# Performance work log

Hardware: AMD Instinct MI355X
Metric: run time of the kernel (lower is better)

The kernel has to match this reference:

```python
import jax, jax.numpy as jnp
import numpy as np

INPUT_DIM = 362
HIDDEN = 256
STYLE_NUM = 60
OUTFIT_NUM = 49710
BATCH = 16384


def setup_inputs() -> dict:
    key = jax.random.key(0)
    ks = jax.random.split(key, 12)
    f32 = jnp.float32
    return {
        "i_feature": jax.random.normal(ks[0], (BATCH, INPUT_DIM), f32),
        "j_feature": jax.random.normal(ks[1], (BATCH, INPUT_DIM), f32),
        "k_feature": jax.random.normal(ks[2], (BATCH, INPUT_DIM), f32),
        # top_emb / bottom_emb Linear params (stored transposed: x @ W + b)
        "W_top": jax.random.normal(ks[3], (INPUT_DIM, HIDDEN), f32) * 0.05,
        "b_top": jnp.zeros((HIDDEN,), f32),
        "W_bot": jax.random.normal(ks[4], (INPUT_DIM, HIDDEN), f32) * 0.05,
        "b_bot": jnp.zeros((HIDDEN,), f32),
        # NMF factors (forward relu_'s them in place; we relu on use)
        "P_nmf": jax.random.normal(ks[5], (2 * INPUT_DIM, STYLE_NUM), f32),
        "N_nmf": jax.random.normal(ks[6], (2 * INPUT_DIM, STYLE_NUM), f32),
        "H1_nmf": jax.random.normal(ks[7], (STYLE_NUM, OUTFIT_NUM), f32),
        "H2_nmf": jax.random.normal(ks[8], (STYLE_NUM, OUTFIT_NUM), f32),
        "matirx_pos": jax.random.uniform(ks[9], (2 * INPUT_DIM, OUTFIT_NUM), f32),
        "matirx_neg": jax.random.uniform(ks[10], (2 * INPUT_DIM, OUTFIT_NUM), f32),
    }


def _emb(x, W, b):
    # nn.Sequential(Linear, Sigmoid)
    return jax.nn.sigmoid(x @ W + b)


def _style_score(i_f, j_f, styles, W_top, b_top, W_bot, b_bot):
    # Vectorized version of the per-sample loop:
    # squared-distance argmin codebook lookup + gather + rowwise dot.
    outfit = jnp.concatenate([i_f, j_f], axis=1)  # [B, 2D]
    # mean over feature dim of (x - s)^2; constant 1/(2D) scale does not change argmin
    d2 = (jnp.sum(outfit * outfit, axis=1, keepdims=True)
          - 2.0 * (outfit @ styles)
          + jnp.sum(styles * styles, axis=0, keepdims=True))  # [B, S]
    idx = jnp.argmin(d2, axis=1)                               # [B]
    sel = styles.T[idx]                                        # [B, 2D] gather
    top, bot = sel[:, :INPUT_DIM], sel[:, INPUT_DIM:]
    # diag(matmul) == rowwise dot
    return jnp.sum(_emb(top, W_top, b_top) * _emb(bot, W_bot, b_bot), axis=1)  # [B]


def reference(i_feature, j_feature, k_feature, W_top, b_top, W_bot, b_bot,
              P_nmf, N_nmf, H1_nmf, H2_nmf, matirx_pos, matirx_neg):
    Ti = _emb(i_feature, W_top, b_top)   # [B, H]
    Bj = _emb(j_feature, W_bot, b_bot)   # [B, H]
    Bk = _emb(k_feature, W_bot, b_bot)   # [B, H]
    # torch.diag(matmul(Ti, Bj.T)) == rowwise dot (avoids [B,B] intermediate)
    ij_score = jnp.sum(Ti * Bj, axis=1)  # [B]
    ik_score = jnp.sum(Ti * Bk, axis=1)  # [B]

    # forward does relu_ on .data before use
    P = jnp.maximum(P_nmf, 0.0)
    N = jnp.maximum(N_nmf, 0.0)
    H1 = jnp.maximum(H1_nmf, 0.0)
    H2 = jnp.maximum(H2_nmf, 0.0)

    style_ij = _style_score(i_feature, j_feature, P, W_top, b_top, W_bot, b_bot)
    style_ik = _style_score(i_feature, k_feature, N, W_top, b_top, W_bot, b_bot)

    # -mean(log(sigmoid(d))) computed stably
    loss1 = -jnp.mean(jax.nn.log_sigmoid(ij_score - ik_score))
    loss2 = -jnp.mean(jax.nn.log_sigmoid(style_ij - style_ik))
    loss3 = jnp.mean(jnp.square(matirx_pos - P @ H1)
                     + jnp.square(matirx_neg - N @ H2))
    loss = loss1 + loss2 + 0.1 * loss3

    ij_ik = jnp.stack([ij_score, ik_score], axis=1)  # [B, 2]
    auc = jnp.mean((jnp.argmax(ij_ik, axis=1) == 0).astype(jnp.float32))
    return (loss, loss1, loss2, loss3, auc)
```

## Files before the change

### kernel.cpp

```cpp
#include <hip/hip_runtime.h>
#include <math.h>

#define BATCH 16384
#define IND   362
#define KP    384
#define HID   256
#define STY   60
#define NOUT  49710
#define OUTP  49920
#define D2    724
#define D2P   768

#define NB_SS   120
#define NB_HR   3120
#define NB_CW   768
#define NB_CPN  384
#define NB_CF   9216
#define NB_PREP (NB_SS + NB_HR + NB_CW + NB_CPN + NB_CF)

#define NB_HH   16
#define NB_PPB  2
#define NB_HEAD (NB_HH + NB_PPB)
#define N_DT    46
#define N_OC    24
#define OCHUNK  2080
#define NB_M    (2 * N_DT * N_OC)
#define NB_EMB  1024
#define NB_SA   512
#define NB_MAIN (NB_HEAD + NB_M + NB_EMB + NB_SA)

typedef __bf16 bf16x8 __attribute__((ext_vector_type(8)));
typedef float  floatx4 __attribute__((ext_vector_type(4)));
typedef float  floatx2 __attribute__((ext_vector_type(2)));

__device__ inline floatx4 mfma16(bf16x8 a, bf16x8 b, floatx4 c) {
  return __builtin_amdgcn_mfma_f32_16x16x32_bf16(a, b, c, 0, 0, 0);
}

__device__ inline unsigned short f32_to_bf16(float x) {
  unsigned int u = __float_as_uint(x);
  unsigned int r = (u + 0x7FFFu + ((u >> 16) & 1u)) >> 16;
  return (unsigned short)r;
}

__device__ inline float sigm_fast(float x) { return 1.0f / (1.0f + __expf(-x)); }
__device__ inline float softplusf(float z) { return fmaxf(z, 0.0f) + log1pf(expf(-fabsf(z))); }

__global__ __launch_bounds__(256) void k_prep(
    const float* __restrict__ fi, const float* __restrict__ fj, const float* __restrict__ fk,
    const float* __restrict__ Wt, const float* __restrict__ btop,
    const float* __restrict__ Wb, const float* __restrict__ bbot,
    const float* __restrict__ Pn, const float* __restrict__ Nn,
    const float* __restrict__ H1, const float* __restrict__ H2,
    unsigned short* __restrict__ fbf, unsigned short* __restrict__ wbfT,
    unsigned short* __restrict__ pnbfT, unsigned short* __restrict__ hrows,
    float* __restrict__ ss, float* __restrict__ cn) {
  __shared__ float sel[D2];
  __shared__ float shr[4];
  int b = blockIdx.x;
  int t = threadIdx.x;

  if (b < NB_SS) {
    int s  = b % STY;
    int mt = b / STY;
    const float* M = mt ? Nn : Pn;
    float cnp = 0.0f;
    for (int d = t; d < D2; d += 256) {
      float v = fmaxf(M[(size_t)d * STY + s], 0.0f);
      sel[d] = v;
      cnp += v * v;
    }
    __syncthreads();
    float at = btop[t], ab = bbot[t];
    for (int d = 0; d < IND; d++) at = fmaf(sel[d],       Wt[(size_t)d * HID + t], at);
    for (int d = 0; d < IND; d++) ab = fmaf(sel[IND + d], Wb[(size_t)d * HID + t], ab);
    float prod = (1.0f / (1.0f + expf(-at))) * (1.0f / (1.0f + expf(-ab)));
    for (int off = 32; off > 0; off >>= 1) prod += __shfl_xor(prod, off);
    if ((t & 63) == 0) shr[t >> 6] = prod;
    __syncthreads();
    if (t == 0) ss[mt * 64 + s] = shr[0] + shr[1] + shr[2] + shr[3];
    __syncthreads();
    for (int off = 32; off > 0; off >>= 1) cnp += __shfl_xor(cnp, off);
    if ((t & 63) == 0) shr[t >> 6] = cnp;
    __syncthreads();
    if (t == 0) cn[mt * 64 + s] = shr[0] + shr[1] + shr[2] + shr[3];
    return;
  }
  b -= NB_SS;

  if (b < NB_HR) {
    int e = (b * 256 + t) * 8;
    int row = e / OUTP;
    int o = e - row * OUTP;
    int s = row & 63;
    int mm = row >> 6;
    const float* H = mm ? H2 : H1;
    unsigned short* dst = hrows + (size_t)row * OUTP + o;
    unsigned int wv[4];
    if (s < STY && o + 8 <= NOUT) {
      const float* src = H + (size_t)s * NOUT + o;
      #pragma unroll
      for (int ee = 0; ee < 4; ee++) {
        floatx2 v = *(const floatx2*)(src + 2 * ee);
        wv[ee] = (unsigned)f32_to_bf16(fmaxf(v[0], 0.0f)) |
                 ((unsigned)f32_to_bf16(fmaxf(v[1], 0.0f)) << 16);
      }
    } else {
      #pragma unroll
      for (int ee = 0; ee < 4; ee++) {
        float lo = (s < STY && o + 2 * ee     < NOUT) ? fmaxf(H[(size_t)s * NOUT + o + 2 * ee],     0.0f) : 0.0f;
        float hi = (s < STY && o + 2 * ee + 1 < NOUT) ? fmaxf(H[(size_t)s * NOUT + o + 2 * ee + 1], 0.0f) : 0.0f;
        wv[ee] = (unsigned)f32_to_bf16(lo) | ((unsigned)f32_to_bf16(hi) << 16);
      }
    }
    uint4 v; v.x = wv[0]; v.y = wv[1]; v.z = wv[2]; v.w = wv[3];
    *(uint4*)dst = v;
    return;
  }
  b -= NB_HR;

  if (b < NB_CW) {
    int idx = b * 256 + t;
    int k = idx % KP;
    int rem = idx / KP;
    int h = rem % HID;
    int mm = rem / HID;
    const float* W = mm ? Wb : Wt;
    wbfT[idx] = f32_to_bf16(k < IND ? W[(size_t)k * HID + h] : 0.0f);
    return;
  }
  b -= NB_CW;

  if (b < NB_CPN) {
    int u = b * 256 + t;
    int s = u & 63;
    int v = u >> 6;
    int m = (v >= D2P) ? 1 : 0;
    int d = v - m * D2P;
    const float* M = m ? Nn : Pn;
    float x = (d < D2 && s < STY) ? fmaxf(M[(size_t)d * STY + s], 0.0f) : 0.0f;
    unsigned short bb = f32_to_bf16(x);
    int k = (d < IND) ? d : (d < D2 ? d + 22 : (d < 746 ? d - IND : d));
    pnbfT[((size_t)m * 64 + s) * D2P + k] = bb;
    return;
  }
  b -= NB_CPN;

  {
    long u = (long)b * 256 + t;
    int g = (int)(u % 48);
    long rf = u / 48;
    int row = (int)(rf % BATCH);
    int f = (int)(rf / BATCH);
    const float* src = (f == 0) ? fi : (f == 1 ? fj : fk);
    int d0 = g * 8;
    const float* sp = src + (size_t)row * IND + d0;
    unsigned int wv[4];
    #pragma unroll
    for (int e = 0; e < 4; e++) {
      int dd = d0 + 2 * e;
      float lo = (dd < IND)     ? sp[2 * e]     : 0.0f;
      float hi = (dd + 1 < IND) ? sp[2 * e + 1] : 0.0f;
      wv[e] = (unsigned)f32_to_bf16(lo) | ((unsigned)f32_to_bf16(hi) << 16);
    }
    uint4 v; v.x = wv[0]; v.y = wv[1]; v.z = wv[2]; v.w = wv[3];
    *(uint4*)(fbf + ((size_t)f * BATCH + row) * KP + d0) = v;
  }
}

__global__ __launch_bounds__(256, 4) void k_main(
    const unsigned short* __restrict__ fbf, const unsigned short* __restrict__ wbfT,
    const unsigned short* __restrict__ pnbfT, const unsigned short* __restrict__ hrows,
    const float* __restrict__ btop, const float* __restrict__ bbot,
    const float* __restrict__ cn, const float* __restrict__ ss,
    const float* __restrict__ mp, const float* __restrict__ mneg,
    const float* __restrict__ Pn, const float* __restrict__ Nn,
    float* __restrict__ sIJ, float* __restrict__ sIK,
    float* __restrict__ stIJ, float* __restrict__ stIK,
    float* __restrict__ HHb, float* __restrict__ PPb,
    float* __restrict__ partial) {
  __shared__ float shp[4];
  __shared__ float red[4096];
  int w = threadIdx.x >> 6, lane = threadIdx.x & 63;
  int m = lane & 15, q = lane >> 4;
  int b = blockIdx.x;

  if (b < NB_HEAD) {
    bool isPP = (b >= NB_HH);
    int mat, chunk, nsteps, stride;
    const unsigned short* Rb;
    if (!isPP) { mat = b >> 3; chunk = b & 7; Rb = hrows + (size_t)mat * 64 * OUTP; stride = OUTP; nsteps = 195; }
    else       { mat = b - NB_HH; chunk = 0; Rb = pnbfT + (size_t)mat * 64 * D2P;  stride = D2P;  nsteps = 24;  }
    const unsigned short* Rm = Rb + (size_t)m * stride;

    floatx4 acc[4][4];
    #pragma unroll
    for (int a2 = 0; a2 < 4; a2++)
      #pragma unroll
      for (int b2 = 0; b2 < 4; b2++) acc[a2][b2] = (floatx4){0.f, 0.f, 0.f, 0.f};

    bf16x8 hc[4], hn[4];
    auto LD = [&](int j, bf16x8* h) {
      int k = (chunk * nsteps + j) * 32 + q * 8;
      #pragma unroll
      for (int st = 0; st < 4; st++)
        h[st] = *(const bf16x8*)(Rm + (size_t)(st * 16) * stride + k);
    };
    int j = w;
    LD(j, hc);
    for (; j < nsteps; j += 4) {
      if (j + 4 < nsteps) LD(j + 4, hn);
      #pragma unroll
      for (int a2 = 0; a2 < 4; a2++)
        #pragma unroll
        for (int b2 = 0; b2 < 4; b2++)
          acc[a2][b2] = mfma16(hc[a2], hc[b2], acc[a2][b2]);
      #pragma unroll
      for (int st = 0; st < 4; st++) hc[st] = hn[st];
    }
    for (int idx = threadIdx.x; idx < 4096; idx += 256) red[idx] = 0.f;
    __syncthreads();
    #pragma unroll
    for (int a2 = 0; a2 < 4; a2++)
      #pragma unroll
      for (int b2 = 0; b2 < 4; b2++)
        #pragma unroll
        for (int r = 0; r < 4; r++)
          atomicAdd(&red[(a2 * 16 + q * 4 + r) * 64 + b2 * 16 + m], acc[a2][b2][r]);
    __syncthreads();
    float* dst = (isPP ? PPb : HHb) + (size_t)mat * 4096;
    for (int idx = threadIdx.x; idx < 4096; idx += 256) atomicAdd(&dst[idx], red[idx]);
    return;
  }
  b -= NB_HEAD;

  if (b < NB_M) {
    int dt  = b % N_DT;
    int r   = b / N_DT;
    int oc  = r % N_OC;
    int mat = r / N_OC;
    int d0 = dt * 16, o0 = oc * OCHUNK;
    bool full = (o0 + OCHUNK <= NOUT);
    int d = d0 + m;
    bool rowok = (d < D2);
    const float* Mrow = (mat ? mneg : mp) + (size_t)d * NOUT;
    const unsigned short* Hbase = hrows + ((size_t)mat * 64 + m) * OUTP;

    floatx4 acc[4];
    #pragma unroll
    for (int st = 0; st < 4; st++) acc[st] = (floatx4){0.f, 0.f, 0.f, 0.f};
    float msq = 0.0f;

    floatx2 mc[4], mnx[4];
    bf16x8  hc[4], hn[4];

    auto LOADM = [&](int j, floatx2* dst) {
      int o = o0 + j * 32 + q * 8;
      if (rowok) {
        const float* Mr = Mrow + o;
        if (full) {
          dst[0] = *(const floatx2*)(Mr);
          dst[1] = *(const floatx2*)(Mr + 2);
          dst[2] = *(const floatx2*)(Mr + 4);
          dst[3] = *(const floatx2*)(Mr + 6);
        } else {
          #pragma unroll
          for (int e = 0; e < 4; e++) {
            floatx2 v = {0.f, 0.f};
            if (o + 2 * e     < NOUT) v[0] = Mr[2 * e];
            if (o + 2 * e + 1 < NOUT) v[1] = Mr[2 * e + 1];
            dst[e] = v;
          }
        }
      } else {
        #pragma unroll
        for (int e = 0; e < 4; e++) dst[e] = (floatx2){0.f, 0.f};
      }
    };
    auto LOADH = [&](int j, bf16x8* h) {
      int o = o0 + j * 32 + q * 8;
      #pragma unroll
      for (int st = 0; st < 4; st++)
        h[st] = *(const bf16x8*)(Hbase + (size_t)(st * 16) * OUTP + o);
    };

    LOADM(w, mc);
    LOADH(w, hc);
    for (int j = w; j < 65; j += 4) {
      if (j + 4 < 65) { LOADM(j + 4, mnx); LOADH(j + 4, hn); }
      union { unsigned int u32[4]; bf16x8 v; } cv;
      #pragma unroll
      for (int e = 0; e < 4; e++) {
        msq = fmaf(mc[e][0], mc[e][0], msq);
        msq = fmaf(mc[e][1], mc[e][1], msq);
        cv.u32[e] = (unsigned)f32_to_bf16(mc[e][0]) | ((unsigned)f32_to_bf16(mc[e][1]) << 16);
      }
      bf16x8 af = cv.v;
      #pragma unroll
      for (int st = 0; st < 4; st++) acc[st] = mfma16(af, hc[st], acc[st]);
      #pragma unroll
      for (int e = 0; e < 4; e++) mc[e] = mnx[e];
      #pragma unroll
      for (int st = 0; st < 4; st++) hc[st] = hn[st];
    }

    const float* PM = mat ? Nn : Pn;
    float t2 = 0.0f;
    #pragma unroll
    for (int st = 0; st < 4; st++) {
      int s = st * 16 + m;
      if (s < STY) {
        #pragma unroll
        for (int rg = 0; rg < 4; rg++) {
          int dd = d0 + q * 4 + rg;
          if (dd < D2) {
            float pv = fmaxf(PM[(size_t)dd * STY + s], 0.0f);
            t2 = fmaf(pv, acc[st][rg], t2);
          }
        }
      }
    }
    float local = msq - 2.0f * t2;
    for (int off = 32; off > 0; off >>= 1) local += __shfl_xor(local, off);
    if (lane == 0) shp[w] = local;
    __syncthreads();
    if (threadIdx.x == 0) partial[b] = shp[0] + shp[1] + shp[2] + shp[3];
    return;
  }
  b -= NB_M;

  if (b < NB_EMB) {
    int r0 = (b & 255) * 64 + w * 16;
    int hb = (b >> 8) * 64;
    const unsigned short* fi = fbf + (size_t)(r0 + m) * KP + q * 8;
    const unsigned short* fj = fi + (size_t)BATCH * KP;
    const unsigned short* fk = fj + (size_t)BATCH * KP;
    floatx4 accI[4], accJ[4], accK[4];
    #pragma unroll
    for (int nt = 0; nt < 4; nt++) {
      accI[nt] = (floatx4){0.f, 0.f, 0.f, 0.f};
      accJ[nt] = (floatx4){0.f, 0.f, 0.f, 0.f};
      accK[nt] = (floatx4){0.f, 0.f, 0.f, 0.f};
    }
    for (int kc = 0; kc < 12; kc++) {
      bf16x8 ai = *(const bf16x8*)(fi + kc * 32);
      bf16x8 aj = *(const bf16x8*)(fj + kc * 32);
      bf16x8 ak = *(const bf16x8*)(fk + kc * 32);
      #pragma unroll
      for (int nt = 0; nt < 4; nt++) {
        int n = hb + nt * 16 + m;
        const unsigned short* wp = wbfT + (size_t)n * KP + kc * 32 + q * 8;
        bf16x8 bt8 = *(const bf16x8*)(wp);
        bf16x8 bb8 = *(const bf16x8*)(wp + (size_t)HID * KP);
        accI[nt] = mfma16(ai, bt8, accI[nt]);
        accJ[nt] = mfma16(aj, bb8, accJ[nt]);
        accK[nt] = mfma16(ak, bb8, accK[nt]);
      }
    }
    float sij[4] = {0.f, 0.f, 0.f, 0.f}, sik[4] = {0.f, 0.f, 0.f, 0.f};
    #pragma unroll
    for (int nt = 0; nt < 4; nt++) {
      int n = hb + nt * 16 + m;
      float vbt = btop[n], vbb = bbot[n];
      #pragma unroll
      for (int reg = 0; reg < 4; reg++) {
        float ti = sigm_fast(accI[nt][reg] + vbt);
        float tj = sigm_fast(accJ[nt][reg] + vbb);
        float tk = sigm_fast(accK[nt][reg] + vbb);
        sij[reg] += ti * tj;
        sik[reg] += ti * tk;
      }
    }
    #pragma unroll
    for (int reg = 0; reg < 4; reg++) {
      for (int off = 1; off < 16; off <<= 1) {
        sij[reg] += __shfl_xor(sij[reg], off);
        sik[reg] += __shfl_xor(sik[reg], off);
      }
    }
    if (m == 0) {
      #pragma unroll
      for (int reg = 0; reg < 4; reg++) {
        int row = r0 + q * 4 + reg;
        atomicAdd(&sIJ[row], sij[reg]);
        atomicAdd(&sIK[row], sik[reg]);
      }
    }
    return;
  }
  b -= NB_EMB;

  {
    int mat = w & 1;
    int r0 = b * 32 + (w >> 1) * 16;
    const unsigned short* fA = fbf + (size_t)(r0 + m) * KP + q * 8;
    const unsigned short* fB = fA + (size_t)(1 + mat) * BATCH * KP;
    const unsigned short* Bp = pnbfT + (size_t)mat * 64 * D2P + q * 8;
    floatx4 acc[4];
    #pragma unroll
    for (int nt = 0; nt < 4; nt++) acc[nt] = (floatx4){0.f, 0.f, 0.f, 0.f};
    for (int kc = 0; kc < 24; kc++) {
      bf16x8 a = (kc < 12) ? *(const bf16x8*)(fA + kc * 32)
                           : *(const bf16x8*)(fB + (kc - 12) * 32);
      #pragma unroll
      for (int nt = 0; nt < 4; nt++) {
        bf16x8 bb = *(const bf16x8*)(Bp + (size_t)(nt * 16 + m) * D2P + kc * 32);
        acc[nt] = mfma16(a, bb, acc[nt]);
      }
    }
    const float* cnm = cn + mat * 64;
    float bv[4]; int bi[4];
    #pragma unroll
    for (int reg = 0; reg < 4; reg++) { bv[reg] = __builtin_inff(); bi[reg] = 1 << 30; }
    #pragma unroll
    for (int nt = 0; nt < 4; nt++) {
      int s = nt * 16 + m;
      float c = cnm[s & 63];
      #pragma unroll
      for (int reg = 0; reg < 4; reg++) {
        float d2 = (s < STY) ? (c - 2.0f * acc[nt][reg]) : __builtin_inff();
        if (d2 < bv[reg] || (d2 == bv[reg] && s < bi[reg])) { bv[reg] = d2; bi[reg] = s; }
      }
    }
    for (int off = 1; off < 16; off <<= 1) {
      #pragma unroll
      for (int reg = 0; reg < 4; reg++) {
        float ov = __shfl_xor(bv[reg], off);
        int   oi = __shfl_xor(bi[reg], off);
        if (ov < bv[reg] || (ov == bv[reg] && oi < bi[reg])) { bv[reg] = ov; bi[reg] = oi; }
      }
    }
    if (m == 0) {
      float* dst = mat ? stIK : stIJ;
      const float* ssm = ss + mat * 64;
      #pragma unroll
      for (int reg = 0; reg < 4; reg++) dst[r0 + q * 4 + reg] = ssm[bi[reg]];
    }
  }
}

__global__ __launch_bounds__(256) void k_final(
    const float* __restrict__ sIJ, const float* __restrict__ sIK,
    const float* __restrict__ stIJ, const float* __restrict__ stIK,
    const float* __restrict__ l3partial,
    const float* __restrict__ HHb, const float* __restrict__ PPb,
    float* __restrict__ out) {
  int t = threadIdx.x;
  float l1 = 0.f, l2 = 0.f, ac = 0.f;
  for (int r = t; r < BATCH; r += 256) {
    float dij = sIJ[r] - sIK[r];
    l1 += softplusf(-dij);
    if (dij >= 0.0f) ac += 1.0f;
    float dst = stIJ[r] - stIK[r];
    l2 += softplusf(-dst);
  }
  double l3 = 0.0;
  for (int p = t; p < NB_M; p += 256) l3 += (double)l3partial[p];
  for (int idx = t; idx < 8192; idx += 256) l3 += (double)HHb[idx] * (double)PPb[idx];
  __shared__ float sh1[4], sh2[4], sh3[4];
  __shared__ double sh4[4];
  for (int off = 32; off > 0; off >>= 1) {
    l1 += __shfl_xor(l1, off);
    l2 += __shfl_xor(l2, off);
    ac += __shfl_xor(ac, off);
    l3 += __shfl_xor(l3, off);
  }
  if ((t & 63) == 0) { sh1[t >> 6] = l1; sh2[t >> 6] = l2; sh3[t >> 6] = ac; sh4[t >> 6] = l3; }
  __syncthreads();
  if (t == 0) {
    double L1 = 0, L2 = 0, AC = 0, L3 = 0;
    for (int i = 0; i < 4; i++) { L1 += sh1[i]; L2 += sh2[i]; AC += sh3[i]; L3 += sh4[i]; }
    L1 /= BATCH; L2 /= BATCH; AC /= BATCH;
    L3 /= ((double)D2 * (double)NOUT);
    out[0] = (float)(L1 + L2 + 0.1 * L3);
    out[1] = (float)L1;
    out[2] = (float)L2;
    out[3] = (float)L3;
    out[4] = (float)AC;
  }
}

extern "C" void kernel_launch(void* const* d_in, const int* in_sizes, int n_in,
                              void* d_out, int out_size, void* d_ws, size_t ws_size,
                              hipStream_t stream) {
  (void)in_sizes; (void)n_in; (void)out_size; (void)ws_size;
  const float* i_f  = (const float*)d_in[0];
  const float* j_f  = (const float*)d_in[1];
  const float* k_f  = (const float*)d_in[2];
  const float* W_t  = (const float*)d_in[3];
  const float* b_t  = (const float*)d_in[4];
  const float* W_b  = (const float*)d_in[5];
  const float* b_b  = (const float*)d_in[6];
  const float* P_n  = (const float*)d_in[7];
  const float* N_n  = (const float*)d_in[8];
  const float* H1   = (const float*)d_in[9];
  const float* H2   = (const float*)d_in[10];
  const float* Mp   = (const float*)d_in[11];
  const float* Mn   = (const float*)d_in[12];
  float* out = (float*)d_out;
  char* ws = (char*)d_ws;

  const size_t OFF_FBF   = 0;
  const size_t OFF_WBFT  = OFF_FBF   + (size_t)3 * BATCH * KP * 2;
  const size_t OFF_PNBFT = OFF_WBFT  + (size_t)2 * HID * KP * 2;
  const size_t OFF_HROWS = OFF_PNBFT + (size_t)2 * 64 * D2P * 2;
  const size_t OFF_SIJ   = OFF_HROWS + (size_t)2 * 64 * OUTP * 2;
  const size_t OFF_SIK   = OFF_SIJ   + (size_t)BATCH * 4;
  const size_t OFF_HH    = OFF_SIK   + (size_t)BATCH * 4;
  const size_t OFF_PP    = OFF_HH    + (size_t)2 * 4096 * 4;
  const size_t OFF_STIJ  = OFF_PP    + (size_t)2 * 4096 * 4;
  const size_t OFF_STIK  = OFF_STIJ  + (size_t)BATCH * 4;
  const size_t OFF_SS    = OFF_STIK  + (size_t)BATCH * 4;
  const size_t OFF_CN    = OFF_SS    + 512;
  const size_t OFF_L3P   = OFF_CN    + 512;

  unsigned short* fbf   = (unsigned short*)(ws + OFF_FBF);
  unsigned short* wbfT  = (unsigned short*)(ws + OFF_WBFT);
  unsigned short* pnbfT = (unsigned short*)(ws + OFF_PNBFT);
  unsigned short* hrows = (unsigned short*)(ws + OFF_HROWS);
  float*  sIJ  = (float*)(ws + OFF_SIJ);
  float*  sIK  = (float*)(ws + OFF_SIK);
  float*  HHb  = (float*)(ws + OFF_HH);
  float*  PPb  = (float*)(ws + OFF_PP);
  float*  stIJ = (float*)(ws + OFF_STIJ);
  float*  stIK = (float*)(ws + OFF_STIK);
  float*  ss   = (float*)(ws + OFF_SS);
  float*  cn   = (float*)(ws + OFF_CN);
  float*  l3p  = (float*)(ws + OFF_L3P);

  hipMemsetAsync(ws + OFF_SIJ, 0, (size_t)BATCH * 4 * 2 + (size_t)4 * 4096 * 4, stream);

  k_prep<<<NB_PREP, 256, 0, stream>>>(i_f, j_f, k_f, W_t, b_t, W_b, b_b,
                                      P_n, N_n, H1, H2,
                                      fbf, wbfT, pnbfT, hrows, ss, cn);
  k_main<<<NB_MAIN, 256, 0, stream>>>(fbf, wbfT, pnbfT, hrows,
                                      b_t, b_b, cn, ss, Mp, Mn, P_n, N_n,
                                      sIJ, sIK, stIJ, stIK, HHb, PPb, l3p);
  k_final<<<1, 256, 0, stream>>>(sIJ, sIK, stIJ, stIK, l3p, HHb, PPb, out);
}
```

Before: 662.8 us.

## Split fused prep/main kernels into per-stage launches and retile the reconstruction loss

The two heterogeneous fused kernels are split into separate launches: conversion, style scores, reconstruction loss, embedding scores, style argmin and the Gram head. The reconstruction-loss kernel is retiled. Output padding goes to 51200 with 2048-wide chunks, each step covers 64 columns in two MFMA sub-steps, and the matrix loads use nontemporal hints. The split removes divergent block roles and register pressure shared across roles, and lets each kernel specialise. The cost is extra launch overhead and the loss of overlap between independent stages within one grid.

```diff
diff --git a/kernel.cpp b/kernel.cpp
--- a/kernel.cpp
+++ b/kernel.cpp
@@ -7,27 +7,29 @@
 #define HID   256
 #define STY   60
 #define NOUT  49710
-#define OUTP  49920
+#define OUTP  51200
 #define D2    724
 #define D2P   768
 
-#define NB_SS   120
-#define NB_HR   3120
+#define NB_HR   3200
 #define NB_CW   768
 #define NB_CPN  384
 #define NB_CF   9216
-#define NB_PREP (NB_SS + NB_HR + NB_CW + NB_CPN + NB_CF)
-
+#define NB_CONV (NB_HR + NB_CW + NB_CPN + NB_CF)
+
+#define NB_SS   120
+
+#define N_DT    46
+#define N_OC    25
+#define OCHUNK  2048
+#define NSTEP_CH 32
+#define NB_M    (2 * N_DT * N_OC)
+
+#define NB_EMB  1024
+#define NB_SA   512
 #define NB_HH   16
 #define NB_PPB  2
 #define NB_HEAD (NB_HH + NB_PPB)
-#define N_DT    46
-#define N_OC    24
-#define OCHUNK  2080
-#define NB_M    (2 * N_DT * N_OC)
-#define NB_EMB  1024
-#define NB_SA   512
-#define NB_MAIN (NB_HEAD + NB_M + NB_EMB + NB_SA)
 
 typedef __bf16 bf16x8 __attribute__((ext_vector_type(8)));
 typedef float  floatx4 __attribute__((ext_vector_type(4)));
@@ -46,47 +48,15 @@
 __device__ inline float sigm_fast(float x) { return 1.0f / (1.0f + __expf(-x)); }
 __device__ inline float softplusf(float z) { return fmaxf(z, 0.0f) + log1pf(expf(-fabsf(z))); }
 
-__global__ __launch_bounds__(256) void k_prep(
+__global__ __launch_bounds__(256) void k_conv(
     const float* __restrict__ fi, const float* __restrict__ fj, const float* __restrict__ fk,
-    const float* __restrict__ Wt, const float* __restrict__ btop,
-    const float* __restrict__ Wb, const float* __restrict__ bbot,
+    const float* __restrict__ Wt, const float* __restrict__ Wb,
     const float* __restrict__ Pn, const float* __restrict__ Nn,
     const float* __restrict__ H1, const float* __restrict__ H2,
     unsigned short* __restrict__ fbf, unsigned short* __restrict__ wbfT,
-    unsigned short* __restrict__ pnbfT, unsigned short* __restrict__ hrows,
-    float* __restrict__ ss, float* __restrict__ cn) {
-  __shared__ float sel[D2];
-  __shared__ float shr[4];
+    unsigned short* __restrict__ pnbfT, unsigned short* __restrict__ hrows) {
   int b = blockIdx.x;
   int t = threadIdx.x;
-
-  if (b < NB_SS) {
-    int s  = b % STY;
-    int mt = b / STY;
-    const float* M = mt ? Nn : Pn;
-    float cnp = 0.0f;
-    for (int d = t; d < D2; d += 256) {
-      float v = fmaxf(M[(size_t)d * STY + s], 0.0f);
-      sel[d] = v;
-      cnp += v * v;
-    }
-    __syncthreads();
-    float at = btop[t], ab = bbot[t];
-    for (int d = 0; d < IND; d++) at = fmaf(sel[d],       Wt[(size_t)d * HID + t], at);
-    for (int d = 0; d < IND; d++) ab = fmaf(sel[IND + d], Wb[(size_t)d * HID + t], ab);
-    float prod = (1.0f / (1.0f + expf(-at))) * (1.0f / (1.0f + expf(-ab)));
-    for (int off = 32; off > 0; off >>= 1) prod += __shfl_xor(prod, off);
-    if ((t & 63) == 0) shr[t >> 6] = prod;
-    __syncthreads();
-    if (t == 0) ss[mt * 64 + s] = shr[0] + shr[1] + shr[2] + shr[3];
-    __syncthreads();
-    for (int off = 32; off > 0; off >>= 1) cnp += __shfl_xor(cnp, off);
-    if ((t & 63) == 0) shr[t >> 6] = cnp;
-    __syncthreads();
-    if (t == 0) cn[mt * 64 + s] = shr[0] + shr[1] + shr[2] + shr[3];
-    return;
-  }
-  b -= NB_SS;
 
   if (b < NB_HR) {
     int e = (b * 256 + t) * 8;
@@ -168,275 +138,317 @@
   }
 }
 
-__global__ __launch_bounds__(256, 4) void k_main(
-    const unsigned short* __restrict__ fbf, const unsigned short* __restrict__ wbfT,
-    const unsigned short* __restrict__ pnbfT, const unsigned short* __restrict__ hrows,
-    const float* __restrict__ btop, const float* __restrict__ bbot,
-    const float* __restrict__ cn, const float* __restrict__ ss,
+__global__ __launch_bounds__(256) void k_style(
+    const float* __restrict__ Wt, const float* __restrict__ btop,
+    const float* __restrict__ Wb, const float* __restrict__ bbot,
+    const float* __restrict__ Pn, const float* __restrict__ Nn,
+    float* __restrict__ ss, float* __restrict__ cn) {
+  __shared__ float sel[D2];
+  __shared__ float shr[4];
+  int b = blockIdx.x;
+  int t = threadIdx.x;
+  int s  = b % STY;
+  int mt = b / STY;
+  const float* M = mt ? Nn : Pn;
+  float cnp = 0.0f;
+  for (int d = t; d < D2; d += 256) {
+    float v = fmaxf(M[(size_t)d * STY + s], 0.0f);
+    sel[d] = v;
+    cnp += v * v;
+  }
+  __syncthreads();
+  float at = btop[t], ab = bbot[t];
+  for (int d = 0; d < IND; d++) at = fmaf(sel[d],       Wt[(size_t)d * HID + t], at);
+  for (int d = 0; d < IND; d++) ab = fmaf(sel[IND + d], Wb[(size_t)d * HID + t], ab);
+  float prod = (1.0f / (1.0f + expf(-at))) * (1.0f / (1.0f + expf(-ab)));
+  for (int off = 32; off > 0; off >>= 1) prod += __shfl_xor(prod, off);
+  if ((t & 63) == 0) shr[t >> 6] = prod;
+  __syncthreads();
+  if (t == 0) ss[mt * 64 + s] = shr[0] + shr[1] + shr[2] + shr[3];
+  __syncthreads();
+  for (int off = 32; off > 0; off >>= 1) cnp += __shfl_xor(cnp, off);
+  if ((t & 63) == 0) shr[t >> 6] = cnp;
+  __syncthreads();
+  if (t == 0) cn[mt * 64 + s] = shr[0] + shr[1] + shr[2] + shr[3];
+}
+
+__global__ __launch_bounds__(256, 4) void k_m(
+    const unsigned short* __restrict__ hrows,
     const float* __restrict__ mp, const float* __restrict__ mneg,
     const float* __restrict__ Pn, const float* __restrict__ Nn,
-    float* __restrict__ sIJ, float* __restrict__ sIK,
-    float* __restrict__ stIJ, float* __restrict__ stIK,
-    float* __restrict__ HHb, float* __restrict__ PPb,
     float* __restrict__ partial) {
   __shared__ float shp[4];
+  int w = threadIdx.x >> 6, lane = threadIdx.x & 63;
+  int m = lane & 15, q = lane >> 4;
+  int b = blockIdx.x;
+  int dt  = b % N_DT;
+  int r   = b / N_DT;
+  int oc  = r % N_OC;
+  int mat = r / N_OC;
+  int d0 = dt * 16, o0 = oc * OCHUNK;
+  bool full = (o0 + OCHUNK <= NOUT);
+  int d = d0 + m;
+  bool rowok = (d < D2);
+  const float* Mrow = (mat ? mneg : mp) + (size_t)d * NOUT;
+  const unsigned short* Hb = hrows + ((size_t)mat * 64 + m) * OUTP;
+
+  floatx4 acc[4];
+  #pragma unroll
+  for (int st = 0; st < 4; st++) acc[st] = (floatx4){0.f, 0.f, 0.f, 0.f};
+  float msq = 0.0f;
+
+  floatx2 mc[8], mn_[8];
+  #pragma unroll
+  for (int e = 0; e < 8; e++) { mc[e] = (floatx2){0.f, 0.f}; mn_[e] = (floatx2){0.f, 0.f}; }
+
+  auto LOADM = [&](int j, floatx2* dst) {
+    if (rowok) {
+      if (full) {
+        #pragma unroll
+        for (int c = 0; c < 2; c++) {
+          const float* Mr = Mrow + o0 + j * 64 + c * 32 + q * 8;
+          dst[c * 4 + 0] = __builtin_nontemporal_load((const floatx2*)(Mr));
+          dst[c * 4 + 1] = __builtin_nontemporal_load((const floatx2*)(Mr + 2));
+          dst[c * 4 + 2] = __builtin_nontemporal_load((const floatx2*)(Mr + 4));
+          dst[c * 4 + 3] = __builtin_nontemporal_load((const floatx2*)(Mr + 6));
+        }
+      } else {
+        #pragma unroll
+        for (int c = 0; c < 2; c++)
+          #pragma unroll
+          for (int e = 0; e < 4; e++) {
+            int o = o0 + j * 64 + c * 32 + q * 8 + 2 * e;
+            floatx2 v = {0.f, 0.f};
+            if (o     < NOUT) v[0] = Mrow[o];
+            if (o + 1 < NOUT) v[1] = Mrow[o + 1];
+            dst[c * 4 + e] = v;
+          }
+      }
+    } else {
+      #pragma unroll
+      for (int e = 0; e < 8; e++) dst[e] = (floatx2){0.f, 0.f};
+    }
+  };
+
+  LOADM(w, mc);
+  for (int j = w; j < NSTEP_CH; j += 4) {
+    if (j + 4 < NSTEP_CH) LOADM(j + 4, mn_);
+    bf16x8 h[2][4];
+    #pragma unroll
+    for (int c = 0; c < 2; c++)
+      #pragma unroll
+      for (int st = 0; st < 4; st++)
+        h[c][st] = *(const bf16x8*)(Hb + (size_t)(st * 16) * OUTP + o0 + j * 64 + c * 32 + q * 8);
+    #pragma unroll
+    for (int c = 0; c < 2; c++) {
+      union { unsigned int u32[4]; bf16x8 v; } cv;
+      #pragma unroll
+      for (int e = 0; e < 4; e++) {
+        floatx2 tv = mc[c * 4 + e];
+        msq = fmaf(tv[0], tv[0], msq);
+        msq = fmaf(tv[1], tv[1], msq);
+        cv.u32[e] = (unsigned)f32_to_bf16(tv[0]) | ((unsigned)f32_to_bf16(tv[1]) << 16);
+      }
+      #pragma unroll
+      for (int st = 0; st < 4; st++) acc[st] = mfma16(cv.v, h[c][st], acc[st]);
+    }
+    #pragma unroll
+    for (int e = 0; e < 8; e++) mc[e] = mn_[e];
+  }
+
+  const float* PM = mat ? Nn : Pn;
+  float t2 = 0.0f;
+  #pragma unroll
+  for (int st = 0; st < 4; st++) {
+    int s = st * 16 + m;
+    if (s < STY) {
+      #pragma unroll
+      for (int rg = 0; rg < 4; rg++) {
+        int dd = d0 + q * 4 + rg;
+        if (dd < D2) {
+          float pv = fmaxf(PM[(size_t)dd * STY + s], 0.0f);
+          t2 = fmaf(pv, acc[st][rg], t2);
+        }
+      }
+    }
+  }
+  float local = msq - 2.0f * t2;
+  for (int off = 32; off > 0; off >>= 1) local += __shfl_xor(local, off);
+  if (lane == 0) shp[w] = local;
+  __syncthreads();
+  if (threadIdx.x == 0) partial[blockIdx.x] = shp[0] + shp[1] + shp[2] + shp[3];
+}
+
+__global__ __launch_bounds__(256, 4) void k_emb(
+    const unsigned short* __restrict__ fbf, const unsigned short* __restrict__ wbfT,
+    const float* __restrict__ btop, const float* __restrict__ bbot,
+    float* __restrict__ sIJ, float* __restrict__ sIK) {
+  int w = threadIdx.x >> 6, lane = threadIdx.x & 63;
+  int m = lane & 15, q = lane >> 4;
+  int b = blockIdx.x;
+  int r0 = (b & 255) * 64 + w * 16;
+  int hb = (b >> 8) * 64;
+  const unsigned short* fi = fbf + (size_t)(r0 + m) * KP + q * 8;
+  const unsigned short* fj = fi + (size_t)BATCH * KP;
+  const unsigned short* fk = fj + (size_t)BATCH * KP;
+  floatx4 accI[4], accJ[4], accK[4];
+  #pragma unroll
+  for (int nt = 0; nt < 4; nt++) {
+    accI[nt] = (floatx4){0.f, 0.f, 0.f, 0.f};
+    accJ[nt] = (floatx4){0.f, 0.f, 0.f, 0.f};
+    accK[nt] = (floatx4){0.f, 0.f, 0.f, 0.f};
+  }
+  for (int kc = 0; kc < 12; kc++) {
+    bf16x8 ai = *(const bf16x8*)(fi + kc * 32);
+    bf16x8 aj = *(const bf16x8*)(fj + kc * 32);
+    bf16x8 ak = *(const bf16x8*)(fk + kc * 32);
+    #pragma unroll
+    for (int nt = 0; nt < 4; nt++) {
+      int n = hb + nt * 16 + m;
+      const unsigned short* wp = wbfT + (size_t)n * KP + kc * 32 + q * 8;
+      bf16x8 bt8 = *(const bf16x8*)(wp);
+      bf16x8 bb8 = *(const bf16x8*)(wp + (size_t)HID * KP);
+      accI[nt] = mfma16(ai, bt8, accI[nt]);
+      accJ[nt] = mfma16(aj, bb8, accJ[nt]);
+      accK[nt] = mfma16(ak, bb8, accK[nt]);
+    }
+  }
+  float sij[4] = {0.f, 0.f, 0.f, 0.f}, sik[4] = {0.f, 0.f, 0.f, 0.f};
+  #pragma unroll
+  for (int nt = 0; nt < 4; nt++) {
+    int n = hb + nt * 16 + m;
+    float vbt = btop[n], vbb = bbot[n];
+    #pragma unroll
+    for (int reg = 0; reg < 4; reg++) {
+      float ti = sigm_fast(accI[nt][reg] + vbt);
+      float tj = sigm_fast(accJ[nt][reg] + vbb);
+      float tk = sigm_fast(accK[nt][reg] + vbb);
+      sij[reg] += ti * tj;
+      sik[reg] += ti * tk;
+    }
+  }
+  #pragma unroll
+  for (int reg = 0; reg < 4; reg++) {
+    for (int off = 1; off < 16; off <<= 1) {
+      sij[reg] += __shfl_xor(sij[reg], off);
+      sik[reg] += __shfl_xor(sik[reg], off);
+    }
+  }
+  if (m == 0) {
+    #pragma unroll
+    for (int reg = 0; reg < 4; reg++) {
+      int row = r0 + q * 4 + reg;
+      atomicAdd(&sIJ[row], sij[reg]);
+      atomicAdd(&sIK[row], sik[reg]);
+    }
+  }
+}
+
+__global__ __launch_bounds__(256, 4) void k_sa(
+    const unsigned short* __restrict__ fbf, const unsigned short* __restrict__ pnbfT,
+    const float* __restrict__ cn, const float* __restrict__ ss,
+    float* __restrict__ stIJ, float* __restrict__ stIK) {
+  int w = threadIdx.x >> 6, lane = threadIdx.x & 63;
+  int m = lane & 15, q = lane >> 4;
+  int b = blockIdx.x;
+  int mat = w & 1;
+  int r0 = b * 32 + (w >> 1) * 16;
+  const unsigned short* fA = fbf + (size_t)(r0 + m) * KP + q * 8;
+  const unsigned short* fB = fA + (size_t)(1 + mat) * BATCH * KP;
+  const unsigned short* Bp = pnbfT + (size_t)mat * 64 * D2P + q * 8;
+  floatx4 acc[4];
+  #pragma unroll
+  for (int nt = 0; nt < 4; nt++) acc[nt] = (floatx4){0.f, 0.f, 0.f, 0.f};
+  for (int kc = 0; kc < 24; kc++) {
+    bf16x8 a = (kc < 12) ? *(const bf16x8*)(fA + kc * 32)
+                         : *(const bf16x8*)(fB + (kc - 12) * 32);
+    #pragma unroll
+    for (int nt = 0; nt < 4; nt++) {
+      bf16x8 bb = *(const bf16x8*)(Bp + (size_t)(nt * 16 + m) * D2P + kc * 32);
+      acc[nt] = mfma16(a, bb, acc[nt]);
+    }
+  }
+  const float* cnm = cn + mat * 64;
+  float bv[4]; int bi[4];
+  #pragma unroll
+  for (int reg = 0; reg < 4; reg++) { bv[reg] = __builtin_inff(); bi[reg] = 1 << 30; }
+  #pragma unroll
+  for (int nt = 0; nt < 4; nt++) {
+    int s = nt * 16 + m;
+    float c = cnm[s & 63];
+    #pragma unroll
+    for (int reg = 0; reg < 4; reg++) {
+      float d2 = (s < STY) ? (c - 2.0f * acc[nt][reg]) : __builtin_inff();
+      if (d2 < bv[reg] || (d2 == bv[reg] && s < bi[reg])) { bv[reg] = d2; bi[reg] = s; }
+    }
+  }
+  for (int off = 1; off < 16; off <<= 1) {
+    #pragma unroll
+    for (int reg = 0; reg < 4; reg++) {
+      float ov = __shfl_xor(bv[reg], off);
+      int   oi = __shfl_xor(bi[reg], off);
+      if (ov < bv[reg] || (ov == bv[reg] && oi < bi[reg])) { bv[reg] = ov; bi[reg] = oi; }
+    }
+  }
+  if (m == 0) {
+    float* dst = mat ? stIK : stIJ;
+    const float* ssm = ss + mat * 64;
+    #pragma unroll
+    for (int reg = 0; reg < 4; reg++) dst[r0 + q * 4 + reg] = ssm[bi[reg]];
+  }
+}
+
+__global__ __launch_bounds__(256) void k_head(
+    const unsigned short* __restrict__ pnbfT, const unsigned short* __restrict__ hrows,
+    float* __restrict__ HHb, float* __restrict__ PPb) {
   __shared__ float red[4096];
   int w = threadIdx.x >> 6, lane = threadIdx.x & 63;
   int m = lane & 15, q = lane >> 4;
   int b = blockIdx.x;
-
-  if (b < NB_HEAD) {
-    bool isPP = (b >= NB_HH);
-    int mat, chunk, nsteps, stride;
-    const unsigned short* Rb;
-    if (!isPP) { mat = b >> 3; chunk = b & 7; Rb = hrows + (size_t)mat * 64 * OUTP; stride = OUTP; nsteps = 195; }
-    else       { mat = b - NB_HH; chunk = 0; Rb = pnbfT + (size_t)mat * 64 * D2P;  stride = D2P;  nsteps = 24;  }
-    const unsigned short* Rm = Rb + (size_t)m * stride;
-
-    floatx4 acc[4][4];
+  bool isPP = (b >= NB_HH);
+  int mat, chunk, nsteps, stride;
+  const unsigned short* Rb;
+  if (!isPP) { mat = b >> 3; chunk = b & 7; Rb = hrows + (size_t)mat * 64 * OUTP; stride = OUTP; nsteps = 200; }
+  else       { mat = b - NB_HH; chunk = 0; Rb = pnbfT + (size_t)mat * 64 * D2P;  stride = D2P;  nsteps = 24;  }
+  const unsigned short* Rm = Rb + (size_t)m * stride;
+
+  floatx4 acc[4][4];
+  #pragma unroll
+  for (int a2 = 0; a2 < 4; a2++)
+    #pragma unroll
+    for (int b2 = 0; b2 < 4; b2++) acc[a2][b2] = (floatx4){0.f, 0.f, 0.f, 0.f};
+
+  bf16x8 hc[4], hn[4];
+  auto LD = [&](int j, bf16x8* h) {
+    int k = (chunk * nsteps + j) * 32 + q * 8;
+    #pragma unroll
+    for (int st = 0; st < 4; st++)
+      h[st] = *(const bf16x8*)(Rm + (size_t)(st * 16) * stride + k);
+  };
+  int j = w;
+  LD(j, hc);
+  for (; j < nsteps; j += 4) {
+    if (j + 4 < nsteps) LD(j + 4, hn);
     #pragma unroll
     for (int a2 = 0; a2 < 4; a2++)
       #pragma unroll
-      for (int b2 = 0; b2 < 4; b2++) acc[a2][b2] = (floatx4){0.f, 0.f, 0.f, 0.f};
-
-    bf16x8 hc[4], hn[4];
-    auto LD = [&](int j, bf16x8* h) {
-      int k = (chunk * nsteps + j) * 32 + q * 8;
-      #pragma unroll
-      for (int st = 0; st < 4; st++)
-        h[st] = *(const bf16x8*)(Rm + (size_t)(st * 16) * stride + k);
-    };
-    int j = w;
-    LD(j, hc);
-    for (; j < nsteps; j += 4) {
-      if (j + 4 < nsteps) LD(j + 4, hn);
-      #pragma unroll
-      for (int a2 = 0; a2 < 4; a2++)
-        #pragma unroll
-        for (int b2 = 0; b2 < 4; b2++)
-          acc[a2][b2] = mfma16(hc[a2], hc[b2], acc[a2][b2]);
-      #pragma unroll
-      for (int st = 0; st < 4; st++) hc[st] = hn[st];
-    }
-    for (int idx = threadIdx.x; idx < 4096; idx += 256) red[idx] = 0.f;
-    __syncthreads();
-    #pragma unroll
-    for (int a2 = 0; a2 < 4; a2++)
-      #pragma unroll
       for (int b2 = 0; b2 < 4; b2++)
-        #pragma unroll
-        for (int r = 0; r < 4; r++)
-          atomicAdd(&red[(a2 * 16 + q * 4 + r) * 64 + b2 * 16 + m], acc[a2][b2][r]);
-    __syncthreads();
-    float* dst = (isPP ? PPb : HHb) + (size_t)mat * 4096;
-    for (int idx = threadIdx.x; idx < 4096; idx += 256) atomicAdd(&dst[idx], red[idx]);
-    return;
-  }
-  b -= NB_HEAD;
-
-  if (b < NB_M) {
-    int dt  = b % N_DT;
-    int r   = b / N_DT;
-    int oc  = r % N_OC;
-    int mat = r / N_OC;
-    int d0 = dt * 16, o0 = oc * OCHUNK;
-    bool full = (o0 + OCHUNK <= NOUT);
-    int d = d0 + m;
-    bool rowok = (d < D2);
-    const float* Mrow = (mat ? mneg : mp) + (size_t)d * NOUT;
-    const unsigned short* Hbase = hrows + ((size_t)mat * 64 + m) * OUTP;
-
-    floatx4 acc[4];
-    #pragma unroll
-    for (int st = 0; st < 4; st++) acc[st] = (floatx4){0.f, 0.f, 0.f, 0.f};
-    float msq = 0.0f;
-
-    floatx2 mc[4], mnx[4];
-    bf16x8  hc[4], hn[4];
-
-    auto LOADM = [&](int j, floatx2* dst) {
-      int o = o0 + j * 32 + q * 8;
-      if (rowok) {
-        const float* Mr = Mrow + o;
-        if (full) {
-          dst[0] = *(const floatx2*)(Mr);
-          dst[1] = *(const floatx2*)(Mr + 2);
-          dst[2] = *(const floatx2*)(Mr + 4);
-          dst[3] = *(const floatx2*)(Mr + 6);
-        } else {
-          #pragma unroll
-          for (int e = 0; e < 4; e++) {
-            floatx2 v = {0.f, 0.f};
-            if (o + 2 * e     < NOUT) v[0] = Mr[2 * e];
-            if (o + 2 * e + 1 < NOUT) v[1] = Mr[2 * e + 1];
-            dst[e] = v;
-          }
-        }
-      } else {
-        #pragma unroll
-        for (int e = 0; e < 4; e++) dst[e] = (floatx2){0.f, 0.f};
-      }
-    };
-    auto LOADH = [&](int j, bf16x8* h) {
-      int o = o0 + j * 32 + q * 8;
-      #pragma unroll
-      for (int st = 0; st < 4; st++)
-        h[st] = *(const bf16x8*)(Hbase + (size_t)(st * 16) * OUTP + o);
-    };
-
-    LOADM(w, mc);
-    LOADH(w, hc);
-    for (int j = w; j < 65; j += 4) {
-      if (j + 4 < 65) { LOADM(j + 4, mnx); LOADH(j + 4, hn); }
-      union { unsigned int u32[4]; bf16x8 v; } cv;
-      #pragma unroll
-      for (int e = 0; e < 4; e++) {
-        msq = fmaf(mc[e][0], mc[e][0], msq);
-        msq = fmaf(mc[e][1], mc[e][1], msq);
-        cv.u32[e] = (unsigned)f32_to_bf16(mc[e][0]) | ((unsigned)f32_to_bf16(mc[e][1]) << 16);
-      }
-      bf16x8 af = cv.v;
-      #pragma unroll
-      for (int st = 0; st < 4; st++) acc[st] = mfma16(af, hc[st], acc[st]);
-      #pragma unroll
-      for (int e = 0; e < 4; e++) mc[e] = mnx[e];
-      #pragma unroll
-      for (int st = 0; st < 4; st++) hc[st] = hn[st];
-    }
-
-    const float* PM = mat ? Nn : Pn;
-    float t2 = 0.0f;
-    #pragma unroll
-    for (int st = 0; st < 4; st++) {
-      int s = st * 16 + m;
-      if (s < STY) {
-        #pragma unroll
-        for (int rg = 0; rg < 4; rg++) {
-          int dd = d0 + q * 4 + rg;
-          if (dd < D2) {
-            float pv = fmaxf(PM[(size_t)dd * STY + s], 0.0f);
-            t2 = fmaf(pv, acc[st][rg], t2);
-          }
-        }
-      }
-    }
-    float local = msq - 2.0f * t2;
-    for (int off = 32; off > 0; off >>= 1) local += __shfl_xor(local, off);
-    if (lane == 0) shp[w] = local;
-    __syncthreads();
-    if (threadIdx.x == 0) partial[b] = shp[0] + shp[1] + shp[2] + shp[3];
-    return;
-  }
-  b -= NB_M;
-
-  if (b < NB_EMB) {
-    int r0 = (b & 255) * 64 + w * 16;
-    int hb = (b >> 8) * 64;
-    const unsigned short* fi = fbf + (size_t)(r0 + m) * KP + q * 8;
-    const unsigned short* fj = fi + (size_t)BATCH * KP;
-    const unsigned short* fk = fj + (size_t)BATCH * KP;
-    floatx4 accI[4], accJ[4], accK[4];
-    #pragma unroll
-    for (int nt = 0; nt < 4; nt++) {
-      accI[nt] = (floatx4){0.f, 0.f, 0.f, 0.f};
-      accJ[nt] = (floatx4){0.f, 0.f, 0.f, 0.f};
-      accK[nt] = (floatx4){0.f, 0.f, 0.f, 0.f};
-    }
-    for (int kc = 0; kc < 12; kc++) {
-      bf16x8 ai = *(const bf16x8*)(fi + kc * 32);
-      bf16x8 aj = *(const bf16x8*)(fj + kc * 32);
-      bf16x8 ak = *(const bf16x8*)(fk + kc * 32);
-      #pragma unroll
-      for (int nt = 0; nt < 4; nt++) {
-        int n = hb + nt * 16 + m;
-        const unsigned short* wp = wbfT + (size_t)n * KP + kc * 32 + q * 8;
-        bf16x8 bt8 = *(const bf16x8*)(wp);
-        bf16x8 bb8 = *(const bf16x8*)(wp + (size_t)HID * KP);
-        accI[nt] = mfma16(ai, bt8, accI[nt]);
-        accJ[nt] = mfma16(aj, bb8, accJ[nt]);
-        accK[nt] = mfma16(ak, bb8, accK[nt]);
-      }
-    }
-    float sij[4] = {0.f, 0.f, 0.f, 0.f}, sik[4] = {0.f, 0.f, 0.f, 0.f};
-    #pragma unroll
-    for (int nt = 0; nt < 4; nt++) {
-      int n = hb + nt * 16 + m;
-      float vbt = btop[n], vbb = bbot[n];
-      #pragma unroll
-      for (int reg = 0; reg < 4; reg++) {
-        float ti = sigm_fast(accI[nt][reg] + vbt);
-        float tj = sigm_fast(accJ[nt][reg] + vbb);
-        float tk = sigm_fast(accK[nt][reg] + vbb);
-        sij[reg] += ti * tj;
-        sik[reg] += ti * tk;
-      }
-    }
-    #pragma unroll
-    for (int reg = 0; reg < 4; reg++) {
-      for (int off = 1; off < 16; off <<= 1) {
-        sij[reg] += __shfl_xor(sij[reg], off);
-        sik[reg] += __shfl_xor(sik[reg], off);
-      }
-    }
-    if (m == 0) {
-      #pragma unroll
-      for (int reg = 0; reg < 4; reg++) {
-        int row = r0 + q * 4 + reg;
-        atomicAdd(&sIJ[row], sij[reg]);
-        atomicAdd(&sIK[row], sik[reg]);
-      }
-    }
-    return;
-  }
-  b -= NB_EMB;
-
-  {
-    int mat = w & 1;
-    int r0 = b * 32 + (w >> 1) * 16;
-    const unsigned short* fA = fbf + (size_t)(r0 + m) * KP + q * 8;
-    const unsigned short* fB = fA + (size_t)(1 + mat) * BATCH * KP;
-    const unsigned short* Bp = pnbfT + (size_t)mat * 64 * D2P + q * 8;
-    floatx4 acc[4];
-    #pragma unroll
-    for (int nt = 0; nt < 4; nt++) acc[nt] = (floatx4){0.f, 0.f, 0.f, 0.f};
-    for (int kc = 0; kc < 24; kc++) {
-      bf16x8 a = (kc < 12) ? *(const bf16x8*)(fA + kc * 32)
-                           : *(const bf16x8*)(fB + (kc - 12) * 32);
-      #pragma unroll
-      for (int nt = 0; nt < 4; nt++) {
-        bf16x8 bb = *(const bf16x8*)(Bp + (size_t)(nt * 16 + m) * D2P + kc * 32);
-        acc[nt] = mfma16(a, bb, acc[nt]);
-      }
-    }
-    const float* cnm = cn + mat * 64;
-    float bv[4]; int bi[4];
-    #pragma unroll
-    for (int reg = 0; reg < 4; reg++) { bv[reg] = __builtin_inff(); bi[reg] = 1 << 30; }
-    #pragma unroll
-    for (int nt = 0; nt < 4; nt++) {
-      int s = nt * 16 + m;
-      float c = cnm[s & 63];
-      #pragma unroll
-      for (int reg = 0; reg < 4; reg++) {
-        float d2 = (s < STY) ? (c - 2.0f * acc[nt][reg]) : __builtin_inff();
-        if (d2 < bv[reg] || (d2 == bv[reg] && s < bi[reg])) { bv[reg] = d2; bi[reg] = s; }
-      }
-    }
-    for (int off = 1; off < 16; off <<= 1) {
-      #pragma unroll
-      for (int reg = 0; reg < 4; reg++) {
-        float ov = __shfl_xor(bv[reg], off);
-        int   oi = __shfl_xor(bi[reg], off);
-        if (ov < bv[reg] || (ov == bv[reg] && oi < bi[reg])) { bv[reg] = ov; bi[reg] = oi; }
-      }
-    }
-    if (m == 0) {
-      float* dst = mat ? stIK : stIJ;
-      const float* ssm = ss + mat * 64;
-      #pragma unroll
-      for (int reg = 0; reg < 4; reg++) dst[r0 + q * 4 + reg] = ssm[bi[reg]];
-    }
-  }
+        acc[a2][b2] = mfma16(hc[a2], hc[b2], acc[a2][b2]);
+    #pragma unroll
+    for (int st = 0; st < 4; st++) hc[st] = hn[st];
+  }
+  for (int idx = threadIdx.x; idx < 4096; idx += 256) red[idx] = 0.f;
+  __syncthreads();
+  #pragma unroll
+  for (int a2 = 0; a2 < 4; a2++)
+    #pragma unroll
+    for (int b2 = 0; b2 < 4; b2++)
+      #pragma unroll
+      for (int r = 0; r < 4; r++)
+        atomicAdd(&red[(a2 * 16 + q * 4 + r) * 64 + b2 * 16 + m], acc[a2][b2][r]);
+  __syncthreads();
+  float* dst = (isPP ? PPb : HHb) + (size_t)mat * 4096;
+  for (int idx = threadIdx.x; idx < 4096; idx += 256) atomicAdd(&dst[idx], red[idx]);
 }
 
 __global__ __launch_bounds__(256) void k_final(
@@ -530,11 +542,12 @@
 
   hipMemsetAsync(ws + OFF_SIJ, 0, (size_t)BATCH * 4 * 2 + (size_t)4 * 4096 * 4, stream);
 
-  k_prep<<<NB_PREP, 256, 0, stream>>>(i_f, j_f, k_f, W_t, b_t, W_b, b_b,
-                                      P_n, N_n, H1, H2,
-                                      fbf, wbfT, pnbfT, hrows, ss, cn);
-  k_main<<<NB_MAIN, 256, 0, stream>>>(fbf, wbfT, pnbfT, hrows,
-                                      b_t, b_b, cn, ss, Mp, Mn, P_n, N_n,
-                                      sIJ, sIK, stIJ, stIK, HHb, PPb, l3p);
+  k_conv<<<NB_CONV, 256, 0, stream>>>(i_f, j_f, k_f, W_t, W_b, P_n, N_n, H1, H2,
+                                      fbf, wbfT, pnbfT, hrows);
+  k_style<<<NB_SS, 256, 0, stream>>>(W_t, b_t, W_b, b_b, P_n, N_n, ss, cn);
+  k_m<<<NB_M, 256, 0, stream>>>(hrows, Mp, Mn, P_n, N_n, l3p);
+  k_emb<<<NB_EMB, 256, 0, stream>>>(fbf, wbfT, b_t, b_b, sIJ, sIK);
+  k_sa<<<NB_SA, 256, 0, stream>>>(fbf, pnbfT, cn, ss, stIJ, stIK);
+  k_head<<<NB_HEAD, 256, 0, stream>>>(pnbfT, hrows, HHb, PPb);
   k_final<<<1, 256, 0, stream>>>(sIJ, sIK, stIJ, stIK, l3p, HHb, PPb, out);
 }
```

Result: slower. 746.7 us (+12.7%).
